# Kernel tuning notes

Hardware: AMD Instinct MI355X
Metric: run time of the kernel (lower is better)

## Reference

```python
import jax, jax.numpy as jnp
import numpy as np

B, T, D = 8, 2048, 1024
HID, OUT, H, WIN = 1024, 512, 4, 9
GAMMA, BIAS_ = 0.6, 0.2


def _window_mask(t, win):
    idx = jnp.clip(jnp.arange(t)[:, None] - win // 2 + jnp.arange(win)[None, :], 0, t - 1)
    return jnp.zeros((t, t), jnp.float32).at[jnp.arange(t)[:, None], idx].set(1.0)


def setup_inputs() -> dict:
    key = jax.random.key(0)
    ks = jax.random.split(key, 10)
    s = lambda d: np.float32(1.0 / np.sqrt(d))
    return {
        'x': jax.random.normal(ks[0], (B, T, D), jnp.float32),
        'seq_len': jax.random.randint(ks[1], (B,), 1, T),
        'Wq': jax.random.normal(ks[2], (D, HID), jnp.float32) * s(D),
        'bq': jnp.zeros((HID,), jnp.float32),
        'Wk': jax.random.normal(ks[3], (D, HID), jnp.float32) * s(D),
        'bk': jnp.zeros((HID,), jnp.float32),
        'Wv': jax.random.normal(ks[4], (D, HID), jnp.float32) * s(D),
        'bv': jnp.zeros((HID,), jnp.float32),
        'Wo': jax.random.normal(ks[5], (HID, D), jnp.float32) * s(HID),
        'bo': jnp.zeros((D,), jnp.float32),
        'ln_g': jnp.ones((D,), jnp.float32),
        'ln_b': jnp.zeros((D,), jnp.float32),
        'W1': jax.random.normal(ks[6], (D // 2, D), jnp.float32) * s(D),   # 1x1 conv d_model -> d_model//2
        'b1': jnp.zeros((D // 2,), jnp.float32),
        'W2': jax.random.normal(ks[7], (OUT, D // 2), jnp.float32) * s(D // 2),  # 1x1 conv -> out_dim
        'b2': jnp.zeros((OUT,), jnp.float32),
        'adj_w': jnp.float32(GAMMA),
        'adj_b': jnp.float32(BIAS_),
    }


def reference(x, seq_len, Wq, bq, Wk, bk, Wv, bv, Wo, bo, ln_g, ln_b, W1, b1, W2, b2, adj_w, adj_b):
    b, t, d = x.shape
    dk = HID // H
    # DistanceAdj: exp(-|w * dist^2 - b|), dist = |i - j|  -> [T, T], broadcast over batch
    dist = jnp.abs(jnp.arange(t)[:, None] - jnp.arange(t)[None, :]).astype(jnp.float32)
    adj = jnp.exp(-jnp.abs(adj_w * dist * dist - adj_b))
    mask = _window_mask(t, WIN)
    # TCA: multi-head attention with window mask + distance-adjacency bias
    q = (x @ Wq + bq).reshape(b, t, H, dk).transpose(0, 2, 1, 3)
    k = (x @ Wk + bk).reshape(b, t, H, dk).transpose(0, 2, 1, 3)
    v = (x @ Wv + bv).reshape(b, t, H, dk).transpose(0, 2, 1, 3)
    scores = jnp.einsum('bhqd,bhkd->bhqk', q, k) / jnp.sqrt(jnp.float32(dk))
    scores = scores + adj[None, None]
    scores = jnp.where(mask[None, None] == 0.0, jnp.float32(-1e9), scores)
    attn = jax.nn.softmax(scores, axis=-1)
    o = jnp.einsum('bhqk,bhkd->bhqd', attn, v).transpose(0, 2, 1, 3).reshape(b, t, HID)
    o = o @ Wo + bo
    # residual + LayerNorm
    y = x + o
    mu = jnp.mean(y, axis=-1, keepdims=True)
    var = jnp.mean((y - mu) ** 2, axis=-1, keepdims=True)
    y = (y - mu) * jax.lax.rsqrt(var + 1e-5) * ln_g + ln_b
    yt = y.transpose(0, 2, 1)  # [B, D, T]
    # 1x1 conv FFN with exact (erf) GELU; dropout is identity in eval
    h1 = jax.nn.gelu(jnp.einsum('od,bdt->bot', W1, yt) + b1[None, :, None], approximate=False)
    xe = jax.nn.gelu(jnp.einsum('oc,bct->bot', W2, h1) + b2[None, :, None], approximate=False)
    return xe, h1
```

## Files before the change

### kernel.cpp

```cpp
#include <hip/hip_runtime.h>
#include <hip/hip_bf16.h>
#include <math.h>

#define B_    8
#define T_    2048
#define D_    1024
#define HID_  1024
#define H_    4
#define DK_   256
#define S_ELEMS ((size_t)16384 * 1024)

typedef __bf16 bf16x8  __attribute__((ext_vector_type(8)));
typedef __bf16 bf16x4v __attribute__((ext_vector_type(4)));
typedef float  f32x4   __attribute__((ext_vector_type(4)));

__device__ __forceinline__ float gelu_f(float x) {
    return 0.5f * x * (1.0f + erff(x * 0.70710678118654752440f));
}

__device__ __forceinline__ void gload_lds16(const void* g, void* s) {
    __builtin_amdgcn_global_load_lds(
        (const __attribute__((address_space(1))) void*)g,
        (__attribute__((address_space(3))) void*)s, 16, 0, 0);
}

template<int EPI>
__global__ __launch_bounds__(512) void gemm256_k(
    const __bf16* __restrict__ A, const __bf16* __restrict__ Bt,
    const float* __restrict__ bias, const __bf16* __restrict__ resb,
    float* __restrict__ Cf, __bf16* __restrict__ Cb,
    int M, int N, int K)
{
    __shared__ __bf16 lds[2][2][256 * 64];
    const int tid = threadIdx.x;
    const int w  = tid >> 6, l = tid & 63;
    const int wm = w >> 2,  wn = w & 3;
    const int lr = l & 15, lq = l >> 4, lx = l & 7;
    const int m0 = blockIdx.x * 256, n0 = blockIdx.y * 256;
    const int nt = K >> 6;

    f32x4 acc[8][4] = {};

    int srow[4], sslot[4];
    #pragma unroll
    for (int c = 0; c < 4; ++c) {
        int i = tid + c * 512;
        srow[c]  = i >> 3;
        sslot[c] = (i & 7) ^ (srow[c] & 7);
    }
    const int ldsu = (w * 64) * 16;

    auto stageA = [&](int t) {
        char* dst = (char*)&lds[t & 1][0][0];
        #pragma unroll
        for (int c = 0; c < 4; ++c)
            gload_lds16((const char*)(A + (size_t)(m0 + srow[c]) * K + t * 64) + (sslot[c] << 4),
                        dst + ldsu + c * 512 * 16);
    };
    auto stageB = [&](int t) {
        char* dst = (char*)&lds[t & 1][1][0];
        #pragma unroll
        for (int c = 0; c < 4; ++c)
            gload_lds16((const char*)(Bt + (size_t)(n0 + srow[c]) * K + t * 64) + (sslot[c] << 4),
                        dst + ldsu + c * 512 * 16);
    };

    stageA(0);
    stageB(0);

    for (int t = 0; t < nt; ++t) {
        const int cur = t & 1;
        if (t + 1 < nt) {
            stageA(t + 1);
            stageB(t + 1);
            asm volatile("s_waitcnt vmcnt(8)" ::: "memory");
        } else {
            asm volatile("s_waitcnt vmcnt(0)" ::: "memory");
        }
        __builtin_amdgcn_s_barrier();
        asm volatile("" ::: "memory");

        const char* Ap = (const char*)&lds[cur][0][0];
        const char* Bp = (const char*)&lds[cur][1][0];

        #pragma unroll
        for (int ks = 0; ks < 2; ++ks) {
            bf16x8 af[8], bfr[4];
            #pragma unroll
            for (int fi = 0; fi < 8; ++fi)
                af[fi] = *(const bf16x8*)(Ap + (wm * 128 + fi * 16 + lr) * 128
                                             + ((((ks << 2) | lq) ^ lx) << 4));
            #pragma unroll
            for (int fj = 0; fj < 4; ++fj)
                bfr[fj] = *(const bf16x8*)(Bp + (wn * 64 + fj * 16 + lr) * 128
                                              + ((((ks << 2) | lq) ^ lx) << 4));
            __builtin_amdgcn_s_setprio(1);
            #pragma unroll
            for (int fi = 0; fi < 8; ++fi)
                #pragma unroll
                for (int fj = 0; fj < 4; ++fj)
                    acc[fi][fj] = __builtin_amdgcn_mfma_f32_16x16x32_bf16(
                        af[fi], bfr[fj], acc[fi][fj], 0, 0, 0);
            __builtin_amdgcn_s_setprio(0);
        }
        __builtin_amdgcn_s_barrier();
        asm volatile("" ::: "memory");
    }

    #pragma unroll
    for (int fi = 0; fi < 8; ++fi) {
        const int row0 = m0 + wm * 128 + fi * 16 + lq * 4;
        #pragma unroll
        for (int fj = 0; fj < 4; ++fj) {
            const int col = n0 + wn * 64 + fj * 16 + lr;
            const float bz = bias[col];
            if (EPI == 0) {
                const int sel = col >> 10, cl = col & 1023;
                __bf16* out = Cb + (size_t)sel * S_ELEMS + (size_t)row0 * 1024 + cl;
                #pragma unroll
                for (int r = 0; r < 4; ++r)
                    out[(size_t)r * 1024] = (__bf16)(acc[fi][fj][r] + bz);
            } else {
                #pragma unroll
                for (int r = 0; r < 4; ++r) {
                    size_t idx = (size_t)(row0 + r) * N + col;
                    Cb[idx] = (__bf16)(acc[fi][fj][r] + bz + (float)resb[idx]);
                }
            }
        }
    }
}

template<int EPI>
__global__ __launch_bounds__(512) void gemmF_k(
    const __bf16* __restrict__ A, const __bf16* __restrict__ Bt,
    const float* __restrict__ bias,
    float* __restrict__ Cf, __bf16* __restrict__ Cb,
    int M, int N, int K)
{
    __shared__ __bf16 lds[2][384 * 64];
    const int tid = threadIdx.x;
    const int w  = tid >> 6, l = tid & 63;
    const int wm = w >> 2,  wn = w & 3;
    const int lr = l & 15, lq = l >> 4, lx = l & 7;
    const int m0 = blockIdx.x * 256, n0 = blockIdx.y * 128;
    const int nt = K >> 6;

    f32x4 acc[8][2] = {};

    int srA[4], ssA[4], srB[2], ssB[2];
    #pragma unroll
    for (int c = 0; c < 4; ++c) {
        int i = tid + c * 512;
        srA[c] = i >> 3;
        ssA[c] = (i & 7) ^ (srA[c] & 7);
    }
    #pragma unroll
    for (int c = 0; c < 2; ++c) {
        int i = tid + c * 512;
        srB[c] = i >> 3;
        ssB[c] = (i & 7) ^ (srB[c] & 7);
    }
    const int ldsu = (w * 64) * 16;

    auto stage = [&](int t) {
        char* dst = (char*)&lds[t & 1][0];
        #pragma unroll
        for (int c = 0; c < 4; ++c)
            gload_lds16((const char*)(A + (size_t)(m0 + srA[c]) * K + t * 64) + (ssA[c] << 4),
                        dst + ldsu + c * 512 * 16);
        char* dstB = dst + 256 * 64 * 2;
        #pragma unroll
        for (int c = 0; c < 2; ++c)
            gload_lds16((const char*)(Bt + (size_t)(n0 + srB[c]) * K + t * 64) + (ssB[c] << 4),
                        dstB + ldsu + c * 512 * 16);
    };

    stage(0);

    for (int t = 0; t < nt; ++t) {
        const int cur = t & 1;
        if (t + 1 < nt) {
            stage(t + 1);
            asm volatile("s_waitcnt vmcnt(6)" ::: "memory");
        } else {
            asm volatile("s_waitcnt vmcnt(0)" ::: "memory");
        }
        __builtin_amdgcn_s_barrier();
        asm volatile("" ::: "memory");

        const char* Ap = (const char*)&lds[cur][0];
        const char* Bp = Ap + 256 * 64 * 2;

        #pragma unroll
        for (int ks = 0; ks < 2; ++ks) {
            bf16x8 af[8], bfr[2];
            #pragma unroll
            for (int fi = 0; fi < 8; ++fi)
                af[fi] = *(const bf16x8*)(Ap + (wm * 128 + fi * 16 + lr) * 128
                                             + ((((ks << 2) | lq) ^ lx) << 4));
            #pragma unroll
            for (int fj = 0; fj < 2; ++fj)
                bfr[fj] = *(const bf16x8*)(Bp + (wn * 32 + fj * 16 + lr) * 128
                                              + ((((ks << 2) | lq) ^ lx) << 4));
            __builtin_amdgcn_s_setprio(1);
            #pragma unroll
            for (int fi = 0; fi < 8; ++fi)
                #pragma unroll
                for (int fj = 0; fj < 2; ++fj)
                    acc[fi][fj] = __builtin_amdgcn_mfma_f32_16x16x32_bf16(
                        af[fi], bfr[fj], acc[fi][fj], 0, 0, 0);
            __builtin_amdgcn_s_setprio(0);
        }
        __builtin_amdgcn_s_barrier();
        asm volatile("" ::: "memory");
    }

    #pragma unroll
    for (int fi = 0; fi < 8; ++fi) {
        const int row0 = m0 + wm * 128 + fi * 16 + lq * 4;
        #pragma unroll
        for (int fj = 0; fj < 2; ++fj) {
            const int col = n0 + wn * 32 + fj * 16 + lr;
            const float bz = bias[col];
            float gv[4];
            #pragma unroll
            for (int r = 0; r < 4; ++r) gv[r] = gelu_f(acc[fi][fj][r] + bz);
            const int bidx = row0 >> 11, t0 = row0 & (T_ - 1);
            f32x4 g4; g4[0] = gv[0]; g4[1] = gv[1]; g4[2] = gv[2]; g4[3] = gv[3];
            __builtin_nontemporal_store(
                g4, (f32x4*)(Cf + (size_t)bidx * N * T_ + (size_t)col * T_ + t0));
            if (EPI == 2) {
                #pragma unroll
                for (int r = 0; r < 4; ++r)
                    Cb[(size_t)(row0 + r) * N + col] = (__bf16)gv[r];
            }
        }
    }
}

__global__ __launch_bounds__(256) void attn4_k(
    const __bf16* Q, const __bf16* __restrict__ Kg, const __bf16* __restrict__ Vg,
    __bf16* O, const float* __restrict__ aw_p, const float* __restrict__ ab_p)
{
    const int tid = threadIdx.x;
    const int s  = tid & 15;
    const int ql = tid >> 4;
    const int b  = blockIdx.x >> 9;
    const int h  = (blockIdx.x >> 7) & 3;
    const int t  = ((blockIdx.x & 127) << 4) + ql;

    const size_t hbase = (size_t)b * T_ * HID_ + h * DK_ + s * 16;

    const __bf16* qp = Q + hbase + (size_t)t * HID_;
    float qf[16];
    #pragma unroll
    for (int c = 0; c < 2; ++c) {
        bf16x8 v = *(const bf16x8*)(qp + c * 8);
        #pragma unroll
        for (int e = 0; e < 8; ++e) qf[c * 8 + e] = (float)v[e];
    }

    float part[9];
    #pragma unroll
    for (int jj = 0; jj < 9; ++jj) {
        int jc = min(max(t - 4 + jj, 0), T_ - 1);
        const __bf16* kp = Kg + hbase + (size_t)jc * HID_;
        float sacc = 0.f;
        #pragma unroll
        for (int c = 0; c < 2; ++c) {
            bf16x8 kv = *(const bf16x8*)(kp + c * 8);
            #pragma unroll
            for (int e = 0; e < 8; ++e) sacc = fmaf(qf[c * 8 + e], (float)kv[e], sacc);
        }
        part[jj] = sacc;
    }

    #pragma unroll
    for (int jj = 0; jj < 9; ++jj) {
        float v = part[jj];
        v += __shfl_xor(v, 1);
        v += __shfl_xor(v, 2);
        v += __shfl_xor(v, 4);
        v += __shfl_xor(v, 8);
        part[jj] = v;
    }

    const float aw = *aw_p, ab = *ab_p;
    float sc[9], mx = -1e30f;
    #pragma unroll
    for (int jj = 0; jj < 9; ++jj) {
        int j = t - 4 + jj;
        float d = (float)(jj - 4);
        float adj = __expf(-fabsf(aw * d * d - ab));
        sc[jj] = (j >= 0 && j < T_) ? part[jj] * (1.0f / 16.0f) + adj : -1e30f;
        mx = fmaxf(mx, sc[jj]);
    }
    float wgt[9], sum = 0.f;
    #pragma unroll
    for (int jj = 0; jj < 9; ++jj) { wgt[jj] = __expf(sc[jj] - mx); sum += wgt[jj]; }
    const float inv = 1.0f / sum;

    float o[16];
    #pragma unroll
    for (int e = 0; e < 16; ++e) o[e] = 0.f;
    #pragma unroll
    for (int jj = 0; jj < 9; ++jj) {
        int jc = min(max(t - 4 + jj, 0), T_ - 1);
        const float wj = wgt[jj] * inv;
        const __bf16* vp = Vg + hbase + (size_t)jc * HID_;
        #pragma unroll
        for (int c = 0; c < 2; ++c) {
            bf16x8 vv = *(const bf16x8*)(vp + c * 8);
            #pragma unroll
            for (int e = 0; e < 8; ++e)
                o[c * 8 + e] = fmaf(wj, (float)vv[e], o[c * 8 + e]);
        }
    }

    __bf16* op = O + hbase + (size_t)t * HID_;
    #pragma unroll
    for (int c = 0; c < 2; ++c) {
        bf16x8 ov;
        #pragma unroll
        for (int e = 0; e < 8; ++e) ov[e] = (__bf16)o[c * 8 + e];
        *(bf16x8*)(op + c * 8) = ov;
    }
}

__device__ __forceinline__ float block_sum(float v, float* sm) {
    #pragma unroll
    for (int off = 32; off; off >>= 1) v += __shfl_xor(v, off);
    if ((threadIdx.x & 63) == 0) sm[threadIdx.x >> 6] = v;
    __syncthreads();
    float r = sm[0] + sm[1] + sm[2] + sm[3];
    __syncthreads();
    return r;
}

__global__ __launch_bounds__(256) void ln_k(
    __bf16* __restrict__ Yb, const float* __restrict__ g, const float* __restrict__ bta)
{
    __shared__ float sm[4];
    __bf16* y = Yb + (size_t)blockIdx.x * D_;
    bf16x4v v4 = *(const bf16x4v*)(y + threadIdx.x * 4);
    float v[4] = { (float)v4[0], (float)v4[1], (float)v4[2], (float)v4[3] };
    float mean = block_sum(v[0] + v[1] + v[2] + v[3], sm) * (1.0f / D_);
    float s2 = 0.f;
    #pragma unroll
    for (int i = 0; i < 4; ++i) { float d = v[i] - mean; s2 += d * d; }
    float rstd = rsqrtf(block_sum(s2, sm) * (1.0f / D_) + 1e-5f);
    bf16x4v o;
    #pragma unroll
    for (int i = 0; i < 4; ++i) {
        int idx = threadIdx.x * 4 + i;
        o[i] = (__bf16)((v[i] - mean) * rstd * g[idx] + bta[idx]);
    }
    *(bf16x4v*)(y + threadIdx.x * 4) = o;
}

__global__ __launch_bounds__(256) void prep_k(
    const float4* __restrict__ x4, const float4* __restrict__ W14,
    const float4* __restrict__ W24,
    const float* __restrict__ bq, const float* __restrict__ bk,
    const float* __restrict__ bv,
    const float* __restrict__ Wq, const float* __restrict__ Wk,
    const float* __restrict__ Wv, const float* __restrict__ Wo,
    bf16x4v* __restrict__ xb4, bf16x4v* __restrict__ W1b4,
    bf16x4v* __restrict__ W2b4, float* __restrict__ bqkvd,
    __bf16* __restrict__ Wqkv, __bf16* __restrict__ Wot)
{
    __shared__ float tbuf[32][33];
    const int bid = blockIdx.x, tid = threadIdx.x;
    if (bid < 16384) {
        int i = bid * 256 + tid;
        float4 v = x4[i];
        bf16x4v o; o[0] = (__bf16)v.x; o[1] = (__bf16)v.y; o[2] = (__bf16)v.z; o[3] = (__bf16)v.w;
        xb4[i] = o;
    } else if (bid < 16896) {
        int i = (bid - 16384) * 256 + tid;
        float4 v = W14[i];
        bf16x4v o; o[0] = (__bf16)v.x; o[1] = (__bf16)v.y; o[2] = (__bf16)v.z; o[3] = (__bf16)v.w;
        W1b4[i] = o;
    } else if (bid < 17152) {
        int i = (bid - 16896) * 256 + tid;
        float4 v = W24[i];
        bf16x4v o; o[0] = (__bf16)v.x; o[1] = (__bf16)v.y; o[2] = (__bf16)v.z; o[3] = (__bf16)v.w;
        W2b4[i] = o;
    } else if (bid < 17164) {
        int i = (bid - 17152) * 256 + tid;
        bqkvd[i] = (i < 1024) ? bq[i] : ((i < 2048) ? bk[i - 1024] : bv[i - 2048]);
    } else {
        int r  = bid - 17164;
        int z  = r >> 10;
        int rt = r & 1023;
        int k0 = ((rt >> 5) & 31) << 5, n0 = (rt & 31) << 5;
        const float* in = (z == 0) ? Wq : (z == 1) ? Wk : (z == 2) ? Wv : Wo;
        __bf16* out = (z < 3) ? (Wqkv + (size_t)z * 1024 * 1024) : Wot;
        int xx = tid & 31, yy = tid >> 5;
        for (int r2 = yy; r2 < 32; r2 += 8)
            tbuf[r2][xx] = in[(size_t)(k0 + r2) * 1024 + n0 + xx];
        __syncthreads();
        for (int r2 = yy; r2 < 32; r2 += 8)
            out[(size_t)(n0 + r2) * 1024 + k0 + xx] = (__bf16)tbuf[xx][r2];
    }
}

extern "C" void kernel_launch(void* const* d_in, const int* in_sizes, int n_in,
                              void* d_out, int out_size, void* d_ws, size_t ws_size,
                              hipStream_t stream) {
    const float* x    = (const float*)d_in[0];
    const float* Wq   = (const float*)d_in[2];
    const float* bq   = (const float*)d_in[3];
    const float* Wk   = (const float*)d_in[4];
    const float* bk   = (const float*)d_in[5];
    const float* Wv   = (const float*)d_in[6];
    const float* bv   = (const float*)d_in[7];
    const float* Wo   = (const float*)d_in[8];
    const float* bo   = (const float*)d_in[9];
    const float* ln_g = (const float*)d_in[10];
    const float* ln_b = (const float*)d_in[11];
    const float* W1   = (const float*)d_in[12];
    const float* b1   = (const float*)d_in[13];
    const float* W2   = (const float*)d_in[14];
    const float* b2   = (const float*)d_in[15];
    const float* adj_w = (const float*)d_in[16];
    const float* adj_b = (const float*)d_in[17];

    const int M = B_ * T_;
    const size_t S = S_ELEMS;

    __bf16* Qb   = (__bf16*)d_ws;
    __bf16* Kb   = Qb + S;
    __bf16* Vb   = Kb + S;
    __bf16* Yb   = Kb;
    __bf16* xb   = Vb + S;
    __bf16* Wqkv = xb + S;
    __bf16* Wot  = Wqkv + 3 * 1024 * 1024;
    __bf16* W1b  = Wot + 1024 * 1024;
    __bf16* W2b  = W1b + 512 * 1024;
    __bf16* h1b  = W2b + 512 * 512;
    float*  bqkvd = (float*)(h1b + (size_t)M * 512);

    float* xe = (float*)d_out;
    float* h1 = xe + (size_t)B_ * 512 * T_;

    dim3 blk(256);

    prep_k<<<dim3(17164 + 4096), blk, 0, stream>>>(
        (const float4*)x, (const float4*)W1, (const float4*)W2, bq, bk, bv,
        Wq, Wk, Wv, Wo,
        (bf16x4v*)xb, (bf16x4v*)W1b, (bf16x4v*)W2b, bqkvd, Wqkv, Wot);

    gemm256_k<0><<<dim3(M / 256, 3072 / 256), dim3(512), 0, stream>>>(
        xb, Wqkv, bqkvd, nullptr, nullptr, Qb, M, 3072, D_);

    attn4_k<<<dim3(B_ * H_ * (T_ / 16)), blk, 0, stream>>>(Qb, Kb, Vb, Qb, adj_w, adj_b);

    gemm256_k<1><<<dim3(M / 256, HID_ / 256), dim3(512), 0, stream>>>(
        Qb, Wot, bo, xb, nullptr, Yb, M, D_, HID_);

    ln_k<<<dim3(M), blk, 0, stream>>>(Yb, ln_g, ln_b);

    gemmF_k<2><<<dim3(M / 256, 512 / 128), dim3(512), 0, stream>>>(
        Yb, W1b, b1, h1, h1b, M, 512, D_);

    gemmF_k<3><<<dim3(M / 256, 512 / 128), dim3(512), 0, stream>>>(
        h1b, W2b, b2, xe, nullptr, M, 512, 512);
}
```

Before: 259.6 us.

## Split GEMM tiles into half-stages and interleave prefetch with four MFMA bursts

Restructures the 256x256 bf16 GEMM main loop so each K-step stages A and B in 128-row halves. Four MFMA bursts, one per quadrant, are interleaved with LDS fragment reads and the async global-to-LDS prefetch of the next step's halves. The aim is finer-grained overlap of memory traffic with matrix math and lower register pressure for fragments. The cost is more barriers per iteration and a changed warp-to-output mapping, so vmcnt waits must still be correct for each half.

```diff
diff --git a/kernel.cpp b/kernel.cpp
--- a/kernel.cpp
+++ b/kernel.cpp
@@ -31,7 +31,7 @@
     float* __restrict__ Cf, __bf16* __restrict__ Cb,
     int M, int N, int K)
 {
-    __shared__ __bf16 lds[2][2][256 * 64];
+    __shared__ __bf16 lds[2][2][2][128 * 64];
     const int tid = threadIdx.x;
     const int w  = tid >> 6, l = tid & 63;
     const int wm = w >> 2,  wn = w & 3;
@@ -41,78 +41,93 @@
 
     f32x4 acc[8][4] = {};
 
-    int srow[4], sslot[4];
-    #pragma unroll
-    for (int c = 0; c < 4; ++c) {
+    int srow[2], sslot[2];
+    #pragma unroll
+    for (int c = 0; c < 2; ++c) {
         int i = tid + c * 512;
         srow[c]  = i >> 3;
         sslot[c] = (i & 7) ^ (srow[c] & 7);
     }
     const int ldsu = (w * 64) * 16;
 
-    auto stageA = [&](int t) {
-        char* dst = (char*)&lds[t & 1][0][0];
-        #pragma unroll
-        for (int c = 0; c < 4; ++c)
-            gload_lds16((const char*)(A + (size_t)(m0 + srow[c]) * K + t * 64) + (sslot[c] << 4),
+    auto stage_half = [&](int t, int hh) {
+        const int ab = hh >> 1, hf = hh & 1;
+        char* dst = (char*)&lds[t & 1][ab][hf][0];
+        const __bf16* src = ab ? Bt : A;
+        const int base0 = ab ? n0 : m0;
+        #pragma unroll
+        for (int c = 0; c < 2; ++c)
+            gload_lds16((const char*)(src + (size_t)(base0 + hf * 128 + srow[c]) * K + t * 64)
+                            + (sslot[c] << 4),
                         dst + ldsu + c * 512 * 16);
     };
-    auto stageB = [&](int t) {
-        char* dst = (char*)&lds[t & 1][1][0];
-        #pragma unroll
-        for (int c = 0; c < 4; ++c)
-            gload_lds16((const char*)(Bt + (size_t)(n0 + srow[c]) * K + t * 64) + (sslot[c] << 4),
-                        dst + ldsu + c * 512 * 16);
-    };
-
-    stageA(0);
-    stageB(0);
-
-    for (int t = 0; t < nt; ++t) {
-        const int cur = t & 1;
-        if (t + 1 < nt) {
-            stageA(t + 1);
-            stageB(t + 1);
-            asm volatile("s_waitcnt vmcnt(8)" ::: "memory");
-        } else {
-            asm volatile("s_waitcnt vmcnt(0)" ::: "memory");
-        }
-        __builtin_amdgcn_s_barrier();
-        asm volatile("" ::: "memory");
-
-        const char* Ap = (const char*)&lds[cur][0][0];
-        const char* Bp = (const char*)&lds[cur][1][0];
-
-        #pragma unroll
-        for (int ks = 0; ks < 2; ++ks) {
-            bf16x8 af[8], bfr[4];
-            #pragma unroll
-            for (int fi = 0; fi < 8; ++fi)
-                af[fi] = *(const bf16x8*)(Ap + (wm * 128 + fi * 16 + lr) * 128
-                                             + ((((ks << 2) | lq) ^ lx) << 4));
-            #pragma unroll
-            for (int fj = 0; fj < 4; ++fj)
-                bfr[fj] = *(const bf16x8*)(Bp + (wn * 64 + fj * 16 + lr) * 128
-                                              + ((((ks << 2) | lq) ^ lx) << 4));
+
+    stage_half(0, 0); stage_half(0, 1); stage_half(0, 2); stage_half(0, 3);
+    asm volatile("s_waitcnt vmcnt(2)" ::: "memory");
+    __builtin_amdgcn_s_barrier();
+    asm volatile("" ::: "memory");
+
+    for (int u = 0; u < nt; ++u) {
+        const int cur = u & 1;
+        const bool pf = (u + 1 < nt);
+
+        bf16x8 af[2][4], b0[2][2], b1[2][2];
+
+        auto rdA = [&](int ah) {
+            const char* Ap = (const char*)&lds[cur][0][ah][0];
+            #pragma unroll
+            for (int ks = 0; ks < 2; ++ks)
+                #pragma unroll
+                for (int fi = 0; fi < 4; ++fi)
+                    af[ks][fi] = *(const bf16x8*)(Ap + (wm * 64 + fi * 16 + lr) * 128
+                                                     + ((((ks << 2) | lq) ^ lx) << 4));
+        };
+        auto rdB = [&](int bh, bf16x8 (&bb)[2][2]) {
+            const char* Bp = (const char*)&lds[cur][1][bh][0];
+            #pragma unroll
+            for (int ks = 0; ks < 2; ++ks)
+                #pragma unroll
+                for (int fj = 0; fj < 2; ++fj)
+                    bb[ks][fj] = *(const bf16x8*)(Bp + (wn * 32 + fj * 16 + lr) * 128
+                                                      + ((((ks << 2) | lq) ^ lx) << 4));
+        };
+        auto burst = [&](int ah, int bh, bf16x8 (&bb)[2][2]) {
+            __builtin_amdgcn_s_barrier();
+            asm volatile("s_waitcnt lgkmcnt(0)" ::: "memory");
             __builtin_amdgcn_s_setprio(1);
             #pragma unroll
-            for (int fi = 0; fi < 8; ++fi)
-                #pragma unroll
-                for (int fj = 0; fj < 4; ++fj)
-                    acc[fi][fj] = __builtin_amdgcn_mfma_f32_16x16x32_bf16(
-                        af[fi], bfr[fj], acc[fi][fj], 0, 0, 0);
+            for (int ks = 0; ks < 2; ++ks)
+                #pragma unroll
+                for (int fi = 0; fi < 4; ++fi)
+                    #pragma unroll
+                    for (int fj = 0; fj < 2; ++fj)
+                        acc[ah * 4 + fi][bh * 2 + fj] = __builtin_amdgcn_mfma_f32_16x16x32_bf16(
+                            af[ks][fi], bb[ks][fj], acc[ah * 4 + fi][bh * 2 + fj], 0, 0, 0);
             __builtin_amdgcn_s_setprio(0);
-        }
-        __builtin_amdgcn_s_barrier();
-        asm volatile("" ::: "memory");
+            __builtin_amdgcn_s_barrier();
+            asm volatile("" ::: "memory");
+        };
+
+        rdA(0); rdB(0, b0);
+        if (pf) { stage_half(u + 1, 0); asm volatile("s_waitcnt vmcnt(2)" ::: "memory"); }
+        else    {                       asm volatile("s_waitcnt vmcnt(0)" ::: "memory"); }
+        burst(0, 0, b0);
+        rdB(1, b1);
+        if (pf) stage_half(u + 1, 1);
+        burst(0, 1, b1);
+        rdA(1);
+        if (pf) stage_half(u + 1, 2);
+        burst(1, 1, b1);
+        if (pf) { stage_half(u + 1, 3); asm volatile("s_waitcnt vmcnt(2)" ::: "memory"); }
+        burst(1, 0, b0);
     }
 
     #pragma unroll
     for (int fi = 0; fi < 8; ++fi) {
-        const int row0 = m0 + wm * 128 + fi * 16 + lq * 4;
+        const int row0 = m0 + (fi >> 2) * 128 + wm * 64 + (fi & 3) * 16 + lq * 4;
         #pragma unroll
         for (int fj = 0; fj < 4; ++fj) {
-            const int col = n0 + wn * 64 + fj * 16 + lr;
+            const int col = n0 + (fj >> 1) * 128 + wn * 32 + (fj & 1) * 16 + lr;
             const float bz = bias[col];
             if (EPI == 0) {
                 const int sel = col >> 10, cl = col & 1023;
```

New measurement: 261.3 us. Within noise of the previous version (+0.7%).
